# Kernel tuning notes

Hardware: AMD Instinct MI355X
Metric: run time of the kernel (lower is better)

Reference implementation:

```python
import jax, jax.numpy as jnp
from jax import lax
import numpy as np

B, IMG_H, IMG_W = 8, 256, 512
NUM_CLASSES, P = 20, 32
SCALE, TOPK, IOU_THR = 32.0, 100, 0.5


def conv2d(x, w, b, stride=1, pad=1):
    y = lax.conv_general_dilated(x, w, (stride, stride), [(pad, pad), (pad, pad)],
                                 dimension_numbers=('NCHW', 'OIHW', 'NCHW'))
    return y + b[None, :, None, None]


def bilinear_resize(img, out_h, out_w):
    # img: [..., H, W]; torch F.interpolate(mode='bilinear', align_corners=False)
    H, W = img.shape[-2], img.shape[-1]
    def idx_w(n_in, n_out):
        src = (jnp.arange(n_out, dtype=jnp.float32) + 0.5) * (n_in / n_out) - 0.5
        src = jnp.clip(src, 0.0, n_in - 1)
        i0 = jnp.floor(src).astype(jnp.int32)
        i1 = jnp.minimum(i0 + 1, n_in - 1)
        return i0, i1, src - i0.astype(jnp.float32)
    y0, y1, wy = idx_w(H, out_h)
    x0, x1, wx = idx_w(W, out_w)
    top = img[..., y0, :] * (1.0 - wy)[:, None] + img[..., y1, :] * wy[:, None]
    return top[..., x0] * (1.0 - wx) + top[..., x1] * wx


def generate_anchors(fh, fw):
    ys = (jnp.arange(fh, dtype=jnp.float32) + 0.5) * (IMG_H / fh)
    xs = (jnp.arange(fw, dtype=jnp.float32) + 0.5) * (IMG_W / fw)
    cy, cx = jnp.meshgrid(ys, xs, indexing='ij')
    h = SCALE / 2
    return jnp.stack([cx - h, cy - h, cx + h, cy + h], -1).reshape(-1, 4)


def delta_to_boxes(anchors, deltas):
    a_c = (anchors[:, :2] + anchors[:, 2:]) / 2
    a_wh = anchors[:, 2:] - anchors[:, :2]
    pc = a_c + deltas[..., :2] * a_wh
    pwh = a_wh * jnp.exp(deltas[..., 2:])
    return jnp.concatenate([pc - pwh / 2, pc + pwh / 2], -1)


def nms_single(boxes, scores, labels):
    # torchvision batched_nms: offset boxes per label, greedy NMS, return kept idxs
    N = boxes.shape[0]
    off = labels.astype(boxes.dtype) * (jnp.max(boxes) + 1.0)
    b = boxes + off[:, None]
    order = jnp.argsort(-scores)
    bs = b[order]
    area = (bs[:, 2] - bs[:, 0]) * (bs[:, 3] - bs[:, 1])
    lt = jnp.maximum(bs[:, None, :2], bs[None, :, :2])
    rb = jnp.minimum(bs[:, None, 2:], bs[None, :, 2:])
    wh = jnp.clip(rb - lt, 0.0)
    inter = wh[..., 0] * wh[..., 1]
    iou = inter / (area[:, None] + area[None, :] - inter + 1e-9)
    idxs = jnp.arange(N)
    def body(i, suppressed):
        keep_i = jnp.logical_not(suppressed[i])
        row = (iou[i] > IOU_THR) & (idxs > i)
        return jnp.where(keep_i, suppressed | row, suppressed)
    suppressed = lax.fori_loop(0, N, body, jnp.zeros(N, bool))
    keep_mask = ~suppressed
    rank = jnp.cumsum(keep_mask) - 1
    slots = jnp.where(keep_mask & (rank < TOPK), rank, TOPK)
    out = jnp.full(TOPK + 1, -1, jnp.int32).at[slots].set(order.astype(jnp.int32))
    return out[:TOPK]


def setup_inputs():
    key = jax.random.key(0)
    ks = jax.random.split(key, 17)
    def cw(k, o, i, kh, kw_):
        return jax.random.normal(k, (o, i, kh, kw_), jnp.float32) / np.sqrt(i * kh * kw_)
    return {
        'images': jax.random.normal(ks[0], (B, 3, IMG_H, IMG_W), jnp.float32),
        'w1': cw(ks[1], 64, 3, 3, 3),   'b1': jnp.zeros(64, jnp.float32),
        'w2': cw(ks[2], 128, 64, 3, 3), 'b2': jnp.zeros(128, jnp.float32),
        'w3': cw(ks[3], 256, 128, 3, 3),'b3': jnp.zeros(256, jnp.float32),
        'pw1': cw(ks[4], 256, 256, 3, 3), 'pb1': jnp.zeros(256, jnp.float32),
        'pw2': cw(ks[5], P, 256, 1, 1),   'pb2': jnp.zeros(P, jnp.float32),
        'cw_': cw(ks[6], NUM_CLASSES + 1, 256, 3, 3), 'cb': jnp.zeros(NUM_CLASSES + 1, jnp.float32),
        'bw': cw(ks[7], 4, 256, 3, 3),  'bb': jnp.zeros(4, jnp.float32),
        'kw': cw(ks[8], P, 256, 3, 3),  'kb': jnp.zeros(P, jnp.float32),
    }


def reference(images, w1, b1, w2, b2, w3, b3, pw1, pb1, pw2, pb2, cw_, cb, bw, bb, kw, kb):
    x = jax.nn.relu(conv2d(images, w1, b1, stride=2))
    x = jax.nn.relu(conv2d(x, w2, b2, stride=2))
    feat = jax.nn.relu(conv2d(x, w3, b3, stride=2))          # [B,256,32,64]
    proto = conv2d(jax.nn.relu(conv2d(feat, pw1, pb1)), pw2, pb2, pad=0)  # [B,P,32,64]
    fh, fw = feat.shape[2], feat.shape[3]
    def head(w, b, c):
        return conv2d(feat, w, b).transpose(0, 2, 3, 1).reshape(B, -1, c)
    cls = head(cw_, cb, NUM_CLASSES + 1)     # [B,N,C+1]
    box = head(bw, bb, 4)                    # [B,N,4]
    coef = head(kw, kb, P)                   # [B,N,P]
    anchors = generate_anchors(fh, fw)       # [N,4]
    probs = jax.nn.softmax(cls, -1)[..., :-1]
    scores = probs.max(-1)
    labels = probs.argmax(-1).astype(jnp.int32)
    boxes = delta_to_boxes(anchors, box)     # [B,N,4]
    keep = jax.vmap(nms_single)(boxes, scores, labels)   # [B,100], -1 pad
    valid = keep >= 0
    ki = jnp.clip(keep, 0)
    take = lambda a: jnp.take_along_axis(a, ki[..., None] if a.ndim == 3 else ki, axis=1)
    boxes_k = take(boxes) * valid[..., None]
    scores_k = take(scores) * valid
    labels_k = jnp.where(valid, take(labels), 0)
    coef_k = jnp.take_along_axis(coef, ki[..., None], axis=1)   # [B,100,P]
    m = jax.nn.sigmoid(jnp.einsum('bkp,bphw->bkhw', coef_k, proto))
    masks = bilinear_resize(m, IMG_H, IMG_W) > 0.5
    masks = masks & valid[..., None, None]
    return boxes_k, scores_k, labels_k, masks, valid
```

## Files before the change

kernel.cpp:

```cpp
#include <hip/hip_runtime.h>
#include <hip/hip_bf16.h>
#include <math.h>

#define BB 8
#define NCLS 21
#define NANCH 2048
#define TOPK_N 100

static const size_t OFF_X1HI = 0;
static const size_t OFF_X1LO = 34344960;
static const size_t OFF_X2HI = 68689920;
static const size_t OFF_X2LO = 86261760;
static const size_t OFF_FTHI = 103833600;
static const size_t OFF_FTLO = 113025024;
static const size_t ZERO_BYTES = 122216448;
static const size_t OFF_WT1  = 122216448;
static const size_t OFF_A2H  = 122223616;
static const size_t OFF_A2L  = 122371072;
static const size_t OFF_A3H  = 122518528;
static const size_t OFF_A3L  = 123108352;
static const size_t OFF_AHH  = 123698176;
static const size_t OFF_AHL  = 123993088;
static const size_t OFF_AP1H = 124288000;
static const size_t OFF_AP1L = 125467648;
static const size_t OFF_WTP2 = 126647296;
static const size_t OFF_BH   = 126680064;
static const size_t OFF_HOUT = 126680576;
static const size_t OFF_P1   = 130874880;
static const size_t OFF_PROTO= 147652096;
static const size_t OFF_BOXES= 149749248;
static const size_t OFF_SCORES=150011392;
static const size_t OFF_LABELS=150076928;
static const size_t OFF_ORDER= 150142464;
static const size_t OFF_SB   = 150208000;
static const size_t OFF_IOU  = 150470144;
static const size_t OFF_KEEP = 154664448;
static const size_t OFF_MAXB = 154668032;
static const size_t OFF_M    = 154668544;

static const size_t OUT_BOXES  = 0;
static const size_t OUT_SCORES = 3200;
static const size_t OUT_LABELS = 4000;
static const size_t OUT_MASKS  = 4800;
static const size_t OUT_VALID  = 104862400;

typedef __attribute__((ext_vector_type(8))) short bf16x8;
typedef __attribute__((ext_vector_type(4))) float f32x4;

__device__ __forceinline__ unsigned encf(float f){
  unsigned u = __float_as_uint(f);
  return (u & 0x80000000u) ? ~u : (u | 0x80000000u);
}
__device__ __forceinline__ float decf(unsigned u){
  unsigned b = (u & 0x80000000u) ? (u & 0x7fffffffu) : ~u;
  return __uint_as_float(b);
}
__device__ __forceinline__ short f2bf(float f){
  __hip_bfloat16 h = __float2bfloat16(f);
  return *(short*)&h;
}
__device__ __forceinline__ float bf2f(short h){
  return __uint_as_float(((unsigned)(unsigned short)h) << 16);
}

__global__ void zerok(float4* __restrict__ p, long n4, unsigned* __restrict__ maxb){
  long i = (long)blockIdx.x*256 + threadIdx.x;
  if (i < BB) maxb[i] = 0u;
  if (i < n4) p[i] = make_float4(0.f,0.f,0.f,0.f);
}

template<int CIN,int COUT,int KK>
__global__ void packw(const float* __restrict__ w, float* __restrict__ wT){
  int i = blockIdx.x*256 + threadIdx.x;
  if (i >= CIN*KK*COUT) return;
  int co = i % COUT; int r = i / COUT;
  int ci = r / KK,  k = r % KK;
  wT[i] = w[(co*CIN + ci)*KK + k];
}

template<int CIN,int COUT>
__global__ void packA(const float* __restrict__ w, short* __restrict__ Ahi,
                      short* __restrict__ Alo){
  constexpr int K = CIN*9;
  constexpr int KS = K/32;
  int i = blockIdx.x*256 + threadIdx.x;
  if (i >= COUT*K) return;
  int sub  = i & 7;
  int lane = (i >> 3) & 63;
  int rest = i >> 9;
  int ks = rest % KS;
  int mt = rest / KS;
  int m = mt*16 + (lane & 15);
  int k = ks*32 + (lane >> 4)*8 + sub;
  int tap = k / CIN, ci = k - tap*CIN;
  float v = w[(m*CIN + ci)*9 + tap];
  short h = f2bf(v);
  Ahi[i] = h;
  Alo[i] = f2bf(v - bf2f(h));
}

__global__ void packAh(const float* __restrict__ cw, const float* __restrict__ bw,
                       const float* __restrict__ kw, const float* __restrict__ cb,
                       const float* __restrict__ bb, const float* __restrict__ kb,
                       short* __restrict__ Ahi, short* __restrict__ Alo,
                       float* __restrict__ bh){
  int i = blockIdx.x*256 + threadIdx.x;
  if (i < 64){
    float v = 0.f;
    if (i < 21) v = cb[i]; else if (i < 25) v = bb[i-21]; else if (i < 57) v = kb[i-25];
    bh[i] = v;
  }
  if (i >= 64*2304) return;
  constexpr int KS = 72;
  int sub  = i & 7;
  int lane = (i >> 3) & 63;
  int rest = i >> 9;
  int ks = rest % KS;
  int mt = rest / KS;
  int m = mt*16 + (lane & 15);
  int k = ks*32 + (lane >> 4)*8 + sub;
  int tap = k >> 8, ci = k & 255;
  float v = 0.f;
  if (m < 21)      v = cw[(m*256 + ci)*9 + tap];
  else if (m < 25) v = bw[((m-21)*256 + ci)*9 + tap];
  else if (m < 57) v = kw[((m-25)*256 + ci)*9 + tap];
  short h = f2bf(v);
  Ahi[i] = h;
  Alo[i] = f2bf(v - bf2f(h));
}

__global__ __launch_bounds__(256) void conv1k(const float* __restrict__ img,
    const float* __restrict__ wT, const float* __restrict__ bias,
    short* __restrict__ x1hi, short* __restrict__ x1lo){
  const int b   = blockIdx.z;
  const int co0 = blockIdx.y * 16;
  const int g   = blockIdx.x*256 + threadIdx.x;
  const int y  = g >> 7;
  const int x0 = (g & 127) << 1;

  float acc[16][2];
#pragma unroll
  for (int c=0;c<16;c++){
    float bv = bias[co0+c];
    acc[c][0] = bv; acc[c][1] = bv;
  }
  int   off[3][5];
  float msk[3][5];
#pragma unroll
  for (int kh=0;kh<3;kh++){
    int iy = y*2 - 1 + kh;
    bool okr = (iy >= 0) && (iy < 256);
    int ro = okr ? iy*512 : 0;
#pragma unroll
    for (int t=0;t<5;t++){
      int col = x0*2 - 1 + t;
      bool ok = okr && (col >= 0) && (col < 512);
      off[kh][t] = ok ? (ro + col) : 0;
      msk[kh][t] = ok ? 1.f : 0.f;
    }
  }
  const float* inb = img + (size_t)b*3*256*512;
  for (int ci=0; ci<3; ci++){
    const float* inc = inb + (size_t)ci*256*512;
    float v[3][5];
#pragma unroll
    for (int kh=0;kh<3;kh++)
#pragma unroll
      for (int t=0;t<5;t++)
        v[kh][t] = inc[off[kh][t]] * msk[kh][t];
    const float* wp = wT + ci*9*64 + co0;
#pragma unroll
    for (int kh=0;kh<3;kh++)
#pragma unroll
    for (int kw=0;kw<3;kw++){
      const float* wq = wp + (kh*3+kw)*64;
#pragma unroll
      for (int c=0;c<16;c++){
        float wv = wq[c];
        acc[c][0] = fmaf(wv, v[kh][2*0+kw], acc[c][0]);
        acc[c][1] = fmaf(wv, v[kh][2*1+kw], acc[c][1]);
      }
    }
  }
#pragma unroll
  for (int s=0;s<2;s++){
    short hv[16] __attribute__((aligned(16)));
    short lv[16] __attribute__((aligned(16)));
#pragma unroll
    for (int c=0;c<16;c++){
      float r = fmaxf(acc[c][s], 0.f);
      short h = f2bf(r);
      hv[c] = h;
      lv[c] = f2bf(r - bf2f(h));
    }
#pragma unroll
    for (int g2=0; g2<2; g2++){
      size_t ad = (((size_t)(b*8 + (co0>>3) + g2)*130 + (y+1))*258 + (x0+s+1))*8;
      *(bf16x8*)(x1hi + ad) = *(bf16x8*)(hv + g2*8);
      *(bf16x8*)(x1lo + ad) = *(bf16x8*)(lv + g2*8);
    }
  }
}

template<int CIN,int K,int M,int MW,int NW,int OW,int OHh,int S,int IPH,int IPW,
         bool SPLIT,int EMODE,int OPH,int OPW>
__global__ __launch_bounds__(NW*64) void cgemm(
    const short* __restrict__ Ahi, const short* __restrict__ Alo,
    const short* __restrict__ Bhi, const short* __restrict__ Blo,
    const float* __restrict__ bias, float* __restrict__ outf,
    short* __restrict__ outhi, short* __restrict__ outlo){
  static_assert(CIN % 32 == 0, "CIN must be multiple of 32");
  constexpr int NT = OW*OHh;
  constexpr int KS = K/32;
  constexpr int CG = CIN/8;
  const int b    = blockIdx.z;
  const int wave = threadIdx.x >> 6;
  const int lane = threadIdx.x & 63;
  const int lm = lane & 15, lq = lane >> 4;
  const int m0 = (blockIdx.y * NW + wave) * (MW*16);
  const int n0 = blockIdx.x * 64;

  int oy[4], ox[4];
#pragma unroll
  for (int j=0;j<4;j++){
    int n = n0 + j*16 + lm;
    oy[j] = n / OW; ox[j] = n % OW;
  }

  f32x4 acc[MW][4];
#pragma unroll
  for (int i=0;i<MW;i++)
#pragma unroll
    for (int j=0;j<4;j++) acc[i][j] = (f32x4){0.f,0.f,0.f,0.f};

  const short* Ah_l = Ahi + (size_t)lane*8;
  const short* Al_l = Alo + (size_t)lane*8;
  const int mt0 = m0 >> 4;

  const size_t plane = (size_t)IPH*IPW;
  const short* Bh0 = Bhi + ((size_t)b*CG + lq)*plane*8;
  const short* Bl0 = Blo + ((size_t)b*CG + lq)*plane*8;

#pragma unroll 3
  for (int tap=0; tap<9; tap++){
    const int dy = tap/3, dx = tap%3;
    size_t pix[4];
#pragma unroll
    for (int j=0;j<4;j++)
      pix[j] = (size_t)(oy[j]*S + dy)*IPW + (size_t)(ox[j]*S + dx);
    const int ksb = tap*(CIN/32);
#pragma unroll
    for (int kc=0; kc<CIN; kc+=32){
      const int ks = ksb + (kc>>5);
      const size_t koff = (size_t)(kc>>3)*plane;
      bf16x8 ah[MW], bh_[4];
#pragma unroll
      for (int i=0;i<MW;i++)
        ah[i] = *(const bf16x8*)(Ah_l + ((size_t)(mt0+i)*KS + ks)*512);
#pragma unroll
      for (int j=0;j<4;j++) bh_[j] = *(const bf16x8*)(Bh0 + (koff + pix[j])*8);
      if constexpr (SPLIT){
        bf16x8 al[MW], bl_[4];
#pragma unroll
        for (int i=0;i<MW;i++)
          al[i] = *(const bf16x8*)(Al_l + ((size_t)(mt0+i)*KS + ks)*512);
#pragma unroll
        for (int j=0;j<4;j++) bl_[j] = *(const bf16x8*)(Bl0 + (koff + pix[j])*8);
#pragma unroll
        for (int j=0;j<4;j++)
#pragma unroll
          for (int i=0;i<MW;i++)
            acc[i][j] = __builtin_amdgcn_mfma_f32_16x16x32_bf16(ah[i], bh_[j], acc[i][j], 0,0,0);
#pragma unroll
        for (int j=0;j<4;j++)
#pragma unroll
          for (int i=0;i<MW;i++)
            acc[i][j] = __builtin_amdgcn_mfma_f32_16x16x32_bf16(ah[i], bl_[j], acc[i][j], 0,0,0);
#pragma unroll
        for (int j=0;j<4;j++)
#pragma unroll
          for (int i=0;i<MW;i++)
            acc[i][j] = __builtin_amdgcn_mfma_f32_16x16x32_bf16(al[i], bh_[j], acc[i][j], 0,0,0);
      } else {
#pragma unroll
        for (int j=0;j<4;j++)
#pragma unroll
          for (int i=0;i<MW;i++)
            acc[i][j] = __builtin_amdgcn_mfma_f32_16x16x32_bf16(ah[i], bh_[j], acc[i][j], 0,0,0);
      }
    }
  }

#pragma unroll
  for (int i=0;i<MW;i++){
#pragma unroll
    for (int r=0;r<4;r++){
      const int m = m0 + i*16 + lq*4 + r;
      const float bv = bias[m];
      if constexpr (EMODE == 0){
#pragma unroll
        for (int j=0;j<4;j++){
          float v = fmaxf(acc[i][j][r] + bv, 0.f);
          short h = f2bf(v);
          short l = f2bf(v - bf2f(h));
          size_t ad = ((((size_t)(b*(M/8) + (m>>3))*OPH + (oy[j]+1))*OPW + (ox[j]+1)))*8 + (m&7);
          outhi[ad] = h;
          outlo[ad] = l;
        }
      } else {
        float* cp = outf + ((size_t)b*M + m)*NT + n0 + lm;
#pragma unroll
        for (int j=0;j<4;j++){
          float v = acc[i][j][r] + bv;
          if constexpr (EMODE == 2) v = fmaxf(v, 0.f);
          cp[j*16] = v;
        }
      }
    }
  }
}

template<int CIN,int K,int M,int MW,int NW,int S,int IPH,int IPW,
         bool SPLIT,int EMODE,int OPH,int OPW>
__global__ __launch_bounds__(NW*64) void cgemm_row(
    const short* __restrict__ Ahi, const short* __restrict__ Alo,
    const short* __restrict__ Bhi, const short* __restrict__ Blo,
    const float* __restrict__ bias, float* __restrict__ outf,
    short* __restrict__ outhi, short* __restrict__ outlo){
  static_assert(CIN % 32 == 0, "CIN must be multiple of 32");
  constexpr int NT = 64*32;
  constexpr int KS = K/32;
  constexpr int CG = CIN/8;
  __shared__ short sB[CG*IPW*8];

  const int b    = blockIdx.z;
  const int oy   = blockIdx.x;
  const int wave = threadIdx.x >> 6;
  const int lane = threadIdx.x & 63;
  const int lm = lane & 15, lq = lane >> 4;
  const int m0 = (blockIdx.y * NW + wave) * (MW*16);
  const int tid = threadIdx.x;

  int ox[4];
#pragma unroll
  for (int j=0;j<4;j++) ox[j] = j*16 + lm;

  f32x4 acc[MW][4];
#pragma unroll
  for (int i=0;i<MW;i++)
#pragma unroll
    for (int j=0;j<4;j++) acc[i][j] = (f32x4){0.f,0.f,0.f,0.f};

  const short* Ah_l = Ahi + (size_t)lane*8;
  const short* Al_l = Alo + (size_t)lane*8;
  const int mt0 = m0 >> 4;
  const size_t plane = (size_t)IPH*IPW;
  const short* Bl0 = Blo + ((size_t)b*CG + lq)*plane*8;

#pragma unroll 1
  for (int dy=0; dy<3; dy++){
    const int iy = oy*S + dy;
    __syncthreads();
    {
      const short* srch = Bhi + ((size_t)b*CG*IPH + iy)*IPW*8;
      for (int c = tid; c < CG*IPW; c += NW*64){
        int g = c / IPW, p = c - g*IPW;
        *(bf16x8*)(&sB[(g*IPW + p)*8]) =
          *(const bf16x8*)(srch + ((size_t)g*plane + p)*8);
      }
    }
    __syncthreads();
#pragma unroll
    for (int dx=0; dx<3; dx++){
      const int tap = dy*3 + dx;
      const int ksb = tap*(CIN/32);
#pragma unroll
      for (int kc=0; kc<CIN; kc+=32){
        const int ks = ksb + (kc>>5);
        bf16x8 ah[MW], bh_[4];
#pragma unroll
        for (int i=0;i<MW;i++)
          ah[i] = *(const bf16x8*)(Ah_l + ((size_t)(mt0+i)*KS + ks)*512);
#pragma unroll
        for (int j=0;j<4;j++){
          int p = ox[j]*S + dx;
          bh_[j] = *(const bf16x8*)(&sB[(((kc>>3) + lq)*IPW + p)*8]);
        }
        if constexpr (SPLIT){
          const size_t koff = (size_t)(kc>>3)*plane;
          bf16x8 al[MW], bl_[4];
#pragma unroll
          for (int i=0;i<MW;i++)
            al[i] = *(const bf16x8*)(Al_l + ((size_t)(mt0+i)*KS + ks)*512);
#pragma unroll
          for (int j=0;j<4;j++){
            size_t pix = (size_t)iy*IPW + (size_t)(ox[j]*S + dx);
            bl_[j] = *(const bf16x8*)(Bl0 + (koff + pix)*8);
          }
#pragma unroll
          for (int j=0;j<4;j++)
#pragma unroll
            for (int i=0;i<MW;i++)
              acc[i][j] = __builtin_amdgcn_mfma_f32_16x16x32_bf16(ah[i], bh_[j], acc[i][j], 0,0,0);
#pragma unroll
          for (int j=0;j<4;j++)
#pragma unroll
            for (int i=0;i<MW;i++)
              acc[i][j] = __builtin_amdgcn_mfma_f32_16x16x32_bf16(ah[i], bl_[j], acc[i][j], 0,0,0);
#pragma unroll
          for (int j=0;j<4;j++)
#pragma unroll
            for (int i=0;i<MW;i++)
              acc[i][j] = __builtin_amdgcn_mfma_f32_16x16x32_bf16(al[i], bh_[j], acc[i][j], 0,0,0);
        } else {
#pragma unroll
          for (int j=0;j<4;j++)
#pragma unroll
            for (int i=0;i<MW;i++)
              acc[i][j] = __builtin_amdgcn_mfma_f32_16x16x32_bf16(ah[i], bh_[j], acc[i][j], 0,0,0);
        }
      }
    }
  }

#pragma unroll
  for (int i=0;i<MW;i++){
#pragma unroll
    for (int r=0;r<4;r++){
      const int m = m0 + i*16 + lq*4 + r;
      const float bv = bias[m];
      if constexpr (EMODE == 0){
#pragma unroll
        for (int j=0;j<4;j++){
          float v = fmaxf(acc[i][j][r] + bv, 0.f);
          short h = f2bf(v);
          short l = f2bf(v - bf2f(h));
          size_t ad = ((((size_t)(b*(M/8) + (m>>3))*OPH + (oy+1))*OPW + (ox[j]+1)))*8 + (m&7);
          outhi[ad] = h;
          outlo[ad] = l;
        }
      } else {
        float* cp = outf + ((size_t)b*M + m)*NT + oy*64 + lm;
#pragma unroll
        for (int j=0;j<4;j++){
          float v = acc[i][j][r] + bv;
          if constexpr (EMODE == 2) v = fmaxf(v, 0.f);
          cp[j*16] = v;
        }
      }
    }
  }
}

__global__ __launch_bounds__(256) void pw2k2(const float* __restrict__ p1,
    const float* __restrict__ wT, const float* __restrict__ bias,
    float* __restrict__ proto){
  const int b  = blockIdx.y;
  const int sp = blockIdx.x*256 + threadIdx.x;
  float acc[32];
#pragma unroll
  for (int c=0;c<32;c++) acc[c] = bias[c];
  const float* pb = p1 + (size_t)b*256*NANCH + sp;
  for (int ci=0;ci<256;ci++){
    float v = pb[(size_t)ci*NANCH];
    const float* wq = wT + ci*32;
#pragma unroll
    for (int c=0;c<32;c++) acc[c] = fmaf(v, wq[c], acc[c]);
  }
#pragma unroll
  for (int c=0;c<32;c++)
    proto[((size_t)b*32 + c)*NANCH + sp] = acc[c];
}

__global__ void decodek(const float* __restrict__ hout,
                        float* __restrict__ boxes, float* __restrict__ scores,
                        int* __restrict__ labels, unsigned* __restrict__ maxb){
  const int b = blockIdx.y;
  const int n = blockIdx.x*blockDim.x + threadIdx.x;
  const float* cp = hout + (size_t)b*64*NANCH + n;
  float l[NCLS];
  float M = -1e30f;
#pragma unroll
  for (int c=0;c<NCLS;c++){ l[c] = cp[(size_t)c*NANCH]; M = fmaxf(M, l[c]); }
  float denom = 0.f;
#pragma unroll
  for (int c=0;c<NCLS;c++) denom += expf(l[c]-M);
  float best = -1.f; int bi = 0;
#pragma unroll
  for (int c=0;c<NCLS-1;c++){
    float e = expf(l[c]-M);
    if (e > best){ best = e; bi = c; }
  }
  scores[(size_t)b*NANCH + n] = best/denom;
  labels[(size_t)b*NANCH + n] = bi;

  float dx = cp[21*(size_t)NANCH], dy = cp[22*(size_t)NANCH];
  float dw = cp[23*(size_t)NANCH], dh = cp[24*(size_t)NANCH];
  const int yy = n >> 6, xx = n & 63;
  float cx = (xx+0.5f)*8.f, cy = (yy+0.5f)*8.f;
  float px = cx + dx*32.f, py = cy + dy*32.f;
  float pw = 32.f*expf(dw), ph = 32.f*expf(dh);
  float x1 = px - 0.5f*pw, y1 = py - 0.5f*ph;
  float x2 = px + 0.5f*pw, y2 = py + 0.5f*ph;
  float* bo = boxes + ((size_t)b*NANCH + n)*4;
  bo[0]=x1; bo[1]=y1; bo[2]=x2; bo[3]=y2;
  float mx = fmaxf(fmaxf(x1,y1), fmaxf(x2,y2));
#pragma unroll
  for (int off=32; off>0; off>>=1) mx = fmaxf(mx, __shfl_down(mx, off));
  if ((threadIdx.x & 63) == 0) atomicMax(maxb + b, encf(mx));
}

__global__ void __launch_bounds__(1024) sortk(const float* __restrict__ scores,
                     const float* __restrict__ boxes, const int* __restrict__ labels,
                     const unsigned* __restrict__ maxb,
                     int* __restrict__ order, float* __restrict__ sb){
  __shared__ float sc[NANCH];
  __shared__ int   id[NANCH];
  const int b = blockIdx.x, t = threadIdx.x;
  for (int i=t;i<NANCH;i+=1024){ sc[i]=scores[(size_t)b*NANCH+i]; id[i]=i; }
  __syncthreads();
  for (int k=2;k<=NANCH;k<<=1){
    for (int j=k>>1;j>0;j>>=1){
      for (int i=t;i<NANCH;i+=1024){
        int ixj = i ^ j;
        if (ixj > i){
          float sa=sc[i], sb_=sc[ixj]; int ia=id[i], ib=id[ixj];
          bool dir = ((i & k) == 0);
          bool before_ba = (sb_ > sa) || (sb_ == sa && ib < ia);
          if (before_ba == dir){ sc[i]=sb_; sc[ixj]=sa; id[i]=ib; id[ixj]=ia; }
        }
      }
      __syncthreads();
    }
  }
  float mboff = decf(maxb[b]) + 1.0f;
  for (int r=t;r<NANCH;r+=1024){
    int o = id[r];
    order[(size_t)b*NANCH + r] = o;
    float off = (float)labels[(size_t)b*NANCH + o] * mboff;
    const float* bo = boxes + ((size_t)b*NANCH + o)*4;
    float* sp = sb + ((size_t)b*NANCH + r)*4;
    sp[0]=bo[0]+off; sp[1]=bo[1]+off; sp[2]=bo[2]+off; sp[3]=bo[3]+off;
  }
}

__global__ void ioumask(const float* __restrict__ sb, unsigned long long* __restrict__ iou){
  const int b = blockIdx.y;
  const int gid = blockIdx.x*blockDim.x + threadIdx.x;
  const int i = gid >> 5, w = gid & 31;
  const float* base = sb + (size_t)b*NANCH*4;
  unsigned long long bits = 0ull;
  const int j0 = w << 6;
  if (j0 + 63 > i){
    float x1=base[i*4], y1=base[i*4+1], x2=base[i*4+2], y2=base[i*4+3];
    float ai = (x2-x1)*(y2-y1);
    for (int jj=0;jj<64;jj++){
      int j = j0 + jj;
      if (j > i){
        float bx1=base[j*4], by1=base[j*4+1], bx2=base[j*4+2], by2=base[j*4+3];
        float lx=fmaxf(x1,bx1), ly=fmaxf(y1,by1);
        float rx=fminf(x2,bx2), ry=fminf(y2,by2);
        float ww=fmaxf(rx-lx,0.f), hh=fmaxf(ry-ly,0.f);
        float inter = ww*hh;
        float aj = (bx2-bx1)*(by2-by1);
        float v = inter/(ai + aj - inter + 1e-9f);
        if (v > 0.5f) bits |= (1ull << jj);
      }
    }
  }
  iou[((size_t)b*NANCH + i)*32 + w] = bits;
}

__global__ void nmsscan(const unsigned long long* __restrict__ iou,
                        const int* __restrict__ order, int* __restrict__ keep){
  const int b = blockIdx.x, lane = threadIdx.x;
  unsigned long long sup = 0ull;
  int k = 0;
  for (int i=0; i<NANCH && k<TOPK_N; i++){
    int wi = i >> 6, bi = i & 63;
    unsigned long long wv = __shfl(sup, wi);
    if (!((wv >> bi) & 1ull)){
      if (lane == 0) keep[b*TOPK_N + k] = order[(size_t)b*NANCH + i];
      k++;
      unsigned long long row = (lane < 32) ? iou[((size_t)b*NANCH + i)*32 + lane] : 0ull;
      sup |= row;
    }
  }
  for (int r = lane; r < TOPK_N; r += 64)
    if (r >= k) keep[b*TOPK_N + r] = -1;
}

__global__ void gatherk(const int* __restrict__ keep, const float* __restrict__ boxes,
                        const float* __restrict__ scores, const int* __restrict__ labels,
                        float* __restrict__ out){
  const int b = blockIdx.x, r = threadIdx.x;
  if (r >= TOPK_N) return;
  int ki = keep[b*TOPK_N + r];
  float valid = (ki >= 0) ? 1.f : 0.f;
  int kc = (ki < 0) ? 0 : ki;
  const float* bo = boxes + ((size_t)b*NANCH + kc)*4;
#pragma unroll
  for (int c=0;c<4;c++) out[OUT_BOXES + ((size_t)b*TOPK_N + r)*4 + c] = bo[c]*valid;
  out[OUT_SCORES + b*TOPK_N + r] = scores[(size_t)b*NANCH + kc]*valid;
  out[OUT_LABELS + b*TOPK_N + r] = (ki >= 0) ? (float)labels[(size_t)b*NANCH + kc] : 0.f;
  out[OUT_VALID  + b*TOPK_N + r] = valid;
}

__global__ void maskm(const int* __restrict__ keep, const float* __restrict__ hout,
                      const float* __restrict__ proto, float* __restrict__ m){
  const int b = blockIdx.z, r = blockIdx.y;
  const int s = blockIdx.x*blockDim.x + threadIdx.x;
  __shared__ float cf[32];
  int ki = keep[b*TOPK_N + r];
  int kc = (ki < 0) ? 0 : ki;
  if (threadIdx.x < 32)
    cf[threadIdx.x] = hout[((size_t)b*64 + 25 + threadIdx.x)*NANCH + kc];
  __syncthreads();
  float acc = 0.f;
#pragma unroll
  for (int p=0;p<32;p++) acc = fmaf(cf[p], proto[((size_t)b*32 + p)*NANCH + s], acc);
  m[((size_t)b*TOPK_N + r)*NANCH + s] = 1.f/(1.f + expf(-acc));
}

__global__ void resizek(const float* __restrict__ m, const int* __restrict__ keep,
                        float* __restrict__ out){
  const int b = blockIdx.z, r = blockIdx.y;
  const int pid = blockIdx.x*blockDim.x + threadIdx.x;
  const int y  = pid >> 7;
  const int x4 = (pid & 127) << 2;
  bool valid = keep[b*TOPK_N + r] >= 0;
  const float* mb = m + ((size_t)b*TOPK_N + r)*NANCH;
  float sy = (y + 0.5f)*0.125f - 0.5f;
  sy = fminf(fmaxf(sy, 0.f), 31.f);
  int y0 = (int)floorf(sy);
  int y1 = min(y0+1, 31);
  float wy = sy - (float)y0;
  const float* r0 = mb + y0*64;
  const float* r1 = mb + y1*64;
  float res[4];
#pragma unroll
  for (int k=0;k<4;k++){
    int x = x4 + k;
    float sx = (x + 0.5f)*0.125f - 0.5f;
    sx = fminf(fmaxf(sx, 0.f), 63.f);
    int x0 = (int)floorf(sx);
    int x1 = min(x0+1, 63);
    float wx = sx - (float)x0;
    float t0 = r0[x0]*(1.f-wy) + r1[x0]*wy;
    float t1 = r0[x1]*(1.f-wy) + r1[x1]*wy;
    float v  = t0*(1.f-wx) + t1*wx;
    res[k] = (v > 0.5f && valid) ? 1.f : 0.f;
  }
  float4 v4 = make_float4(res[0], res[1], res[2], res[3]);
  *(float4*)(out + OUT_MASKS + (((size_t)b*TOPK_N + r)*256 + y)*512 + x4) = v4;
}

extern "C" void kernel_launch(void* const* d_in, const int* in_sizes, int n_in,
                              void* d_out, int out_size, void* d_ws, size_t ws_size,
                              hipStream_t stream) {
  const float* images=(const float*)d_in[0];
  const float* w1=(const float*)d_in[1];  const float* b1=(const float*)d_in[2];
  const float* w2=(const float*)d_in[3];  const float* b2=(const float*)d_in[4];
  const float* w3=(const float*)d_in[5];  const float* b3=(const float*)d_in[6];
  const float* pw1=(const float*)d_in[7]; const float* pb1=(const float*)d_in[8];
  const float* pw2=(const float*)d_in[9]; const float* pb2=(const float*)d_in[10];
  const float* cw=(const float*)d_in[11]; const float* cb=(const float*)d_in[12];
  const float* bw=(const float*)d_in[13]; const float* bb=(const float*)d_in[14];
  const float* kw=(const float*)d_in[15]; const float* kb=(const float*)d_in[16];
  float* out = (float*)d_out;
  char* ws = (char*)d_ws;

  short* x1hi = (short*)(ws + OFF_X1HI);
  short* x1lo = (short*)(ws + OFF_X1LO);
  short* x2hi = (short*)(ws + OFF_X2HI);
  short* x2lo = (short*)(ws + OFF_X2LO);
  short* fthi = (short*)(ws + OFF_FTHI);
  short* ftlo = (short*)(ws + OFF_FTLO);
  float* wT1  = (float*)(ws + OFF_WT1);
  short* a2h  = (short*)(ws + OFF_A2H);
  short* a2l  = (short*)(ws + OFF_A2L);
  short* a3h  = (short*)(ws + OFF_A3H);
  short* a3l  = (short*)(ws + OFF_A3L);
  short* ahh  = (short*)(ws + OFF_AHH);
  short* ahl  = (short*)(ws + OFF_AHL);
  short* ap1h = (short*)(ws + OFF_AP1H);
  short* ap1l = (short*)(ws + OFF_AP1L);
  float* wTp2 = (float*)(ws + OFF_WTP2);
  float* bh   = (float*)(ws + OFF_BH);
  float* hout = (float*)(ws + OFF_HOUT);
  float* p1   = (float*)(ws + OFF_P1);
  float* proto= (float*)(ws + OFF_PROTO);
  float* boxes= (float*)(ws + OFF_BOXES);
  float* scores=(float*)(ws + OFF_SCORES);
  int*   labels=(int*)  (ws + OFF_LABELS);
  int*   order =(int*)  (ws + OFF_ORDER);
  float* sb   = (float*)(ws + OFF_SB);
  unsigned long long* iou = (unsigned long long*)(ws + OFF_IOU);
  int*   keep = (int*)  (ws + OFF_KEEP);
  unsigned* maxb = (unsigned*)(ws + OFF_MAXB);
  float* m    = (float*)(ws + OFF_M);

  zerok<<<dim3((unsigned)(ZERO_BYTES/16/256)), 256, 0, stream>>>((float4*)ws, (long)(ZERO_BYTES/16), maxb);

  packw<3,64,9>  <<<dim3(7),    256, 0, stream>>>(w1, wT1);
  packA<64,128>  <<<dim3(288),  256, 0, stream>>>(w2, a2h, a2l);
  packA<128,256> <<<dim3(1152), 256, 0, stream>>>(w3, a3h, a3l);
  packA<256,256> <<<dim3(2304), 256, 0, stream>>>(pw1, ap1h, ap1l);
  packAh<<<dim3(576), 256, 0, stream>>>(cw, bw, kw, cb, bb, kb, ahh, ahl, bh);
  packw<256,32,1><<<dim3(32),   256, 0, stream>>>(pw2, wTp2);

  conv1k<<<dim3(64,4,BB), 256, 0, stream>>>(images, wT1, b1, x1hi, x1lo);

  cgemm<64,576,128,2,4,128,64,2,130,258,true,0,66,130>
      <<<dim3(128,1,BB), 256, 0, stream>>>(a2h, a2l, x1hi, x1lo, b2, nullptr, x2hi, x2lo);

  cgemm_row<128,1152,256,2,4,2,66,130,true,0,34,66>
      <<<dim3(32,2,BB), 256, 0, stream>>>(a3h, a3l, x2hi, x2lo, b3, nullptr, fthi, ftlo);

  cgemm_row<256,2304,64,2,2,1,34,66,true,1,1,1>
      <<<dim3(32,1,BB), 128, 0, stream>>>(ahh, ahl, fthi, ftlo, bh, hout, nullptr, nullptr);

  cgemm_row<256,2304,256,2,4,1,34,66,false,2,1,1>
      <<<dim3(32,2,BB), 256, 0, stream>>>(ap1h, ap1l, fthi, fthi, pb1, p1, nullptr, nullptr);

  pw2k2<<<dim3(8,BB), 256, 0, stream>>>(p1, wTp2, pb2, proto);

  decodek<<<dim3(8,BB), 256, 0, stream>>>(hout, boxes, scores, labels, maxb);
  sortk<<<dim3(BB), 1024, 0, stream>>>(scores, boxes, labels, maxb, order, sb);
  ioumask<<<dim3(256,BB), 256, 0, stream>>>(sb, iou);
  nmsscan<<<dim3(BB), 64, 0, stream>>>(iou, order, keep);
  gatherk<<<dim3(BB), 128, 0, stream>>>(keep, boxes, scores, labels, out);

  maskm<<<dim3(8,TOPK_N,BB), 256, 0, stream>>>(keep, hout, proto, m);
  resizek<<<dim3(128,TOPK_N,BB), 256, 0, stream>>>(m, keep, out);
}
```

Measured before the change: 1.004 ms.

## Zero only halos, stage lo planes in LDS, unify conv GEMMs, skip invalid masks

```diff
diff --git a/kernel.cpp b/kernel.cpp
--- a/kernel.cpp
+++ b/kernel.cpp
@@ -13,7 +13,6 @@
 static const size_t OFF_X2LO = 86261760;
 static const size_t OFF_FTHI = 103833600;
 static const size_t OFF_FTLO = 113025024;
-static const size_t ZERO_BYTES = 122216448;
 static const size_t OFF_WT1  = 122216448;
 static const size_t OFF_A2H  = 122223616;
 static const size_t OFF_A2L  = 122371072;
@@ -63,10 +62,22 @@
   return __uint_as_float(((unsigned)(unsigned short)h) << 16);
 }
 
-__global__ void zerok(float4* __restrict__ p, long n4, unsigned* __restrict__ maxb){
-  long i = (long)blockIdx.x*256 + threadIdx.x;
-  if (i < BB) maxb[i] = 0u;
-  if (i < n4) p[i] = make_float4(0.f,0.f,0.f,0.f);
+template<int CH8,int Hp,int Wp>
+__global__ void halok(short* __restrict__ hi, short* __restrict__ lo,
+                      unsigned* __restrict__ maxb){
+  constexpr int PER = 2*Wp + 2*(Hp-2);
+  int i = blockIdx.x*256 + threadIdx.x;
+  if (maxb && i < BB) maxb[i] = 0u;
+  if (i >= BB*CH8*PER) return;
+  int cell = i % PER; int bg = i / PER;
+  int y, x;
+  if (cell < Wp)        { y = 0;      x = cell; }
+  else if (cell < 2*Wp) { y = Hp-1;   x = cell - Wp; }
+  else { int r = cell - 2*Wp; y = 1 + (r>>1); x = (r&1) ? (Wp-1) : 0; }
+  size_t ad = (((size_t)bg*Hp + y)*Wp + x)*8;
+  bf16x8 z = (bf16x8){0,0,0,0,0,0,0,0};
+  *(bf16x8*)(hi + ad) = z;
+  *(bf16x8*)(lo + ad) = z;
 }
 
 template<int CIN,int COUT,int KK>
@@ -202,149 +213,34 @@
   }
 }
 
-template<int CIN,int K,int M,int MW,int NW,int OW,int OHh,int S,int IPH,int IPW,
-         bool SPLIT,int EMODE,int OPH,int OPW>
-__global__ __launch_bounds__(NW*64) void cgemm(
-    const short* __restrict__ Ahi, const short* __restrict__ Alo,
-    const short* __restrict__ Bhi, const short* __restrict__ Blo,
-    const float* __restrict__ bias, float* __restrict__ outf,
-    short* __restrict__ outhi, short* __restrict__ outlo){
-  static_assert(CIN % 32 == 0, "CIN must be multiple of 32");
-  constexpr int NT = OW*OHh;
-  constexpr int KS = K/32;
-  constexpr int CG = CIN/8;
-  const int b    = blockIdx.z;
-  const int wave = threadIdx.x >> 6;
-  const int lane = threadIdx.x & 63;
-  const int lm = lane & 15, lq = lane >> 4;
-  const int m0 = (blockIdx.y * NW + wave) * (MW*16);
-  const int n0 = blockIdx.x * 64;
-
-  int oy[4], ox[4];
-#pragma unroll
-  for (int j=0;j<4;j++){
-    int n = n0 + j*16 + lm;
-    oy[j] = n / OW; ox[j] = n % OW;
-  }
-
-  f32x4 acc[MW][4];
-#pragma unroll
-  for (int i=0;i<MW;i++)
-#pragma unroll
-    for (int j=0;j<4;j++) acc[i][j] = (f32x4){0.f,0.f,0.f,0.f};
-
-  const short* Ah_l = Ahi + (size_t)lane*8;
-  const short* Al_l = Alo + (size_t)lane*8;
-  const int mt0 = m0 >> 4;
-
-  const size_t plane = (size_t)IPH*IPW;
-  const short* Bh0 = Bhi + ((size_t)b*CG + lq)*plane*8;
-  const short* Bl0 = Blo + ((size_t)b*CG + lq)*plane*8;
-
-#pragma unroll 3
-  for (int tap=0; tap<9; tap++){
-    const int dy = tap/3, dx = tap%3;
-    size_t pix[4];
-#pragma unroll
-    for (int j=0;j<4;j++)
-      pix[j] = (size_t)(oy[j]*S + dy)*IPW + (size_t)(ox[j]*S + dx);
-    const int ksb = tap*(CIN/32);
-#pragma unroll
-    for (int kc=0; kc<CIN; kc+=32){
-      const int ks = ksb + (kc>>5);
-      const size_t koff = (size_t)(kc>>3)*plane;
-      bf16x8 ah[MW], bh_[4];
-#pragma unroll
-      for (int i=0;i<MW;i++)
-        ah[i] = *(const bf16x8*)(Ah_l + ((size_t)(mt0+i)*KS + ks)*512);
-#pragma unroll
-      for (int j=0;j<4;j++) bh_[j] = *(const bf16x8*)(Bh0 + (koff + pix[j])*8);
-      if constexpr (SPLIT){
-        bf16x8 al[MW], bl_[4];
-#pragma unroll
-        for (int i=0;i<MW;i++)
-          al[i] = *(const bf16x8*)(Al_l + ((size_t)(mt0+i)*KS + ks)*512);
-#pragma unroll
-        for (int j=0;j<4;j++) bl_[j] = *(const bf16x8*)(Bl0 + (koff + pix[j])*8);
-#pragma unroll
-        for (int j=0;j<4;j++)
-#pragma unroll
-          for (int i=0;i<MW;i++)
-            acc[i][j] = __builtin_amdgcn_mfma_f32_16x16x32_bf16(ah[i], bh_[j], acc[i][j], 0,0,0);
-#pragma unroll
-        for (int j=0;j<4;j++)
-#pragma unroll
-          for (int i=0;i<MW;i++)
-            acc[i][j] = __builtin_amdgcn_mfma_f32_16x16x32_bf16(ah[i], bl_[j], acc[i][j], 0,0,0);
-#pragma unroll
-        for (int j=0;j<4;j++)
-#pragma unroll
-          for (int i=0;i<MW;i++)
-            acc[i][j] = __builtin_amdgcn_mfma_f32_16x16x32_bf16(al[i], bh_[j], acc[i][j], 0,0,0);
-      } else {
-#pragma unroll
-        for (int j=0;j<4;j++)
-#pragma unroll
-          for (int i=0;i<MW;i++)
-            acc[i][j] = __builtin_amdgcn_mfma_f32_16x16x32_bf16(ah[i], bh_[j], acc[i][j], 0,0,0);
-      }
-    }
-  }
-
-#pragma unroll
-  for (int i=0;i<MW;i++){
-#pragma unroll
-    for (int r=0;r<4;r++){
-      const int m = m0 + i*16 + lq*4 + r;
-      const float bv = bias[m];
-      if constexpr (EMODE == 0){
-#pragma unroll
-        for (int j=0;j<4;j++){
-          float v = fmaxf(acc[i][j][r] + bv, 0.f);
-          short h = f2bf(v);
-          short l = f2bf(v - bf2f(h));
-          size_t ad = ((((size_t)(b*(M/8) + (m>>3))*OPH + (oy[j]+1))*OPW + (ox[j]+1)))*8 + (m&7);
-          outhi[ad] = h;
-          outlo[ad] = l;
-        }
-      } else {
-        float* cp = outf + ((size_t)b*M + m)*NT + n0 + lm;
-#pragma unroll
-        for (int j=0;j<4;j++){
-          float v = acc[i][j][r] + bv;
-          if constexpr (EMODE == 2) v = fmaxf(v, 0.f);
-          cp[j*16] = v;
-        }
-      }
-    }
-  }
-}
-
-template<int CIN,int K,int M,int MW,int NW,int S,int IPH,int IPW,
-         bool SPLIT,int EMODE,int OPH,int OPW>
+template<int CIN,int K,int M,int MW,int NW,int S,int IPH,int IPW,int NXB,
+         bool SPLIT,bool STAGELO,int EMODE,int OPH,int OPW>
 __global__ __launch_bounds__(NW*64) void cgemm_row(
     const short* __restrict__ Ahi, const short* __restrict__ Alo,
     const short* __restrict__ Bhi, const short* __restrict__ Blo,
     const float* __restrict__ bias, float* __restrict__ outf,
     short* __restrict__ outhi, short* __restrict__ outlo){
   static_assert(CIN % 32 == 0, "CIN must be multiple of 32");
+  static_assert(EMODE == 0 || NXB == 1, "flat out assumes OW=64");
   constexpr int NT = 64*32;
   constexpr int KS = K/32;
   constexpr int CG = CIN/8;
-  __shared__ short sB[CG*IPW*8];
+  constexpr int SW  = 64*S + 2;
+  constexpr int SWP = (S==2) ? (SW/2 + 1) : SW;
+  constexpr int PARS = (S==2) ? 2 : 1;
+  constexpr int LOOFF = CG*PARS*SWP*8;
+  constexpr int BUFS = (SPLIT && STAGELO) ? 2 : 1;
+  __shared__ __align__(16) short sB[BUFS*LOOFF];
 
   const int b    = blockIdx.z;
-  const int oy   = blockIdx.x;
+  const int oy   = blockIdx.x / NXB;
+  const int xb   = (blockIdx.x % NXB) * 64;
   const int wave = threadIdx.x >> 6;
   const int lane = threadIdx.x & 63;
   const int lm = lane & 15, lq = lane >> 4;
   const int m0 = (blockIdx.y * NW + wave) * (MW*16);
   const int tid = threadIdx.x;
 
-  int ox[4];
-#pragma unroll
-  for (int j=0;j<4;j++) ox[j] = j*16 + lm;
-
   f32x4 acc[MW][4];
 #pragma unroll
   for (int i=0;i<MW;i++)
@@ -362,11 +258,21 @@
     const int iy = oy*S + dy;
     __syncthreads();
     {
-      const short* srch = Bhi + ((size_t)b*CG*IPH + iy)*IPW*8;
-      for (int c = tid; c < CG*IPW; c += NW*64){
-        int g = c / IPW, p = c - g*IPW;
-        *(bf16x8*)(&sB[(g*IPW + p)*8]) =
+      const short* srch = Bhi + (((size_t)b*CG*IPH + iy)*IPW + (size_t)(xb*S))*8;
+      for (int c = tid; c < CG*SW; c += NW*64){
+        int g = c / SW, p = c - g*SW;
+        int dst = (S==2) ? ((g*2 + (p&1))*SWP + (p>>1)) : (g*SW + p);
+        *(bf16x8*)(&sB[(size_t)dst*8]) =
           *(const bf16x8*)(srch + ((size_t)g*plane + p)*8);
+      }
+      if constexpr (SPLIT && STAGELO){
+        const short* srcl = Blo + (((size_t)b*CG*IPH + iy)*IPW + (size_t)(xb*S))*8;
+        for (int c = tid; c < CG*SW; c += NW*64){
+          int g = c / SW, p = c - g*SW;
+          int dst = (S==2) ? ((g*2 + (p&1))*SWP + (p>>1)) : (g*SW + p);
+          *(bf16x8*)(&sB[LOOFF + (size_t)dst*8]) =
+            *(const bf16x8*)(srcl + ((size_t)g*plane + p)*8);
+        }
       }
     }
     __syncthreads();
@@ -374,28 +280,37 @@
     for (int dx=0; dx<3; dx++){
       const int tap = dy*3 + dx;
       const int ksb = tap*(CIN/32);
-#pragma unroll
       for (int kc=0; kc<CIN; kc+=32){
         const int ks = ksb + (kc>>5);
+        int ra[4];
+#pragma unroll
+        for (int j=0;j<4;j++){
+          int pc = (j*16 + lm)*S + dx;
+          ra[j] = (S==2) ? ((((kc>>3) + lq)*2 + (pc&1))*SWP + (pc>>1))
+                         : (((kc>>3) + lq)*SW + pc);
+        }
         bf16x8 ah[MW], bh_[4];
 #pragma unroll
         for (int i=0;i<MW;i++)
           ah[i] = *(const bf16x8*)(Ah_l + ((size_t)(mt0+i)*KS + ks)*512);
 #pragma unroll
-        for (int j=0;j<4;j++){
-          int p = ox[j]*S + dx;
-          bh_[j] = *(const bf16x8*)(&sB[(((kc>>3) + lq)*IPW + p)*8]);
-        }
+        for (int j=0;j<4;j++)
+          bh_[j] = *(const bf16x8*)(&sB[(size_t)ra[j]*8]);
         if constexpr (SPLIT){
-          const size_t koff = (size_t)(kc>>3)*plane;
           bf16x8 al[MW], bl_[4];
 #pragma unroll
           for (int i=0;i<MW;i++)
             al[i] = *(const bf16x8*)(Al_l + ((size_t)(mt0+i)*KS + ks)*512);
-#pragma unroll
-          for (int j=0;j<4;j++){
-            size_t pix = (size_t)iy*IPW + (size_t)(ox[j]*S + dx);
-            bl_[j] = *(const bf16x8*)(Bl0 + (koff + pix)*8);
+          if constexpr (STAGELO){
+#pragma unroll
+            for (int j=0;j<4;j++)
+              bl_[j] = *(const bf16x8*)(&sB[LOOFF + (size_t)ra[j]*8]);
+          } else {
+#pragma unroll
+            for (int j=0;j<4;j++){
+              size_t pix = (size_t)iy*IPW + (size_t)((xb + j*16 + lm)*S + dx);
+              bl_[j] = *(const bf16x8*)(Bl0 + ((size_t)(kc>>3)*plane + pix)*8);
+            }
           }
 #pragma unroll
           for (int j=0;j<4;j++)
@@ -432,10 +347,11 @@
       if constexpr (EMODE == 0){
 #pragma unroll
         for (int j=0;j<4;j++){
+          const int ox = xb + j*16 + lm;
           float v = fmaxf(acc[i][j][r] + bv, 0.f);
           short h = f2bf(v);
           short l = f2bf(v - bf2f(h));
-          size_t ad = ((((size_t)(b*(M/8) + (m>>3))*OPH + (oy+1))*OPW + (ox[j]+1)))*8 + (m&7);
+          size_t ad = ((((size_t)(b*(M/8) + (m>>3))*OPH + (oy+1))*OPW + (ox+1)))*8 + (m&7);
           outhi[ad] = h;
           outlo[ad] = l;
         }
@@ -609,12 +525,12 @@
 __global__ void maskm(const int* __restrict__ keep, const float* __restrict__ hout,
                       const float* __restrict__ proto, float* __restrict__ m){
   const int b = blockIdx.z, r = blockIdx.y;
+  int ki = keep[b*TOPK_N + r];
+  if (ki < 0) return;
   const int s = blockIdx.x*blockDim.x + threadIdx.x;
   __shared__ float cf[32];
-  int ki = keep[b*TOPK_N + r];
-  int kc = (ki < 0) ? 0 : ki;
   if (threadIdx.x < 32)
-    cf[threadIdx.x] = hout[((size_t)b*64 + 25 + threadIdx.x)*NANCH + kc];
+    cf[threadIdx.x] = hout[((size_t)b*64 + 25 + threadIdx.x)*NANCH + ki];
   __syncthreads();
   float acc = 0.f;
 #pragma unroll
@@ -628,7 +544,12 @@
   const int pid = blockIdx.x*blockDim.x + threadIdx.x;
   const int y  = pid >> 7;
   const int x4 = (pid & 127) << 2;
+  float* dst = out + OUT_MASKS + (((size_t)b*TOPK_N + r)*256 + y)*512 + x4;
   bool valid = keep[b*TOPK_N + r] >= 0;
+  if (!valid){
+    *(float4*)dst = make_float4(0.f,0.f,0.f,0.f);
+    return;
+  }
   const float* mb = m + ((size_t)b*TOPK_N + r)*NANCH;
   float sy = (y + 0.5f)*0.125f - 0.5f;
   sy = fminf(fmaxf(sy, 0.f), 31.f);
@@ -649,10 +570,9 @@
     float t0 = r0[x0]*(1.f-wy) + r1[x0]*wy;
     float t1 = r0[x1]*(1.f-wy) + r1[x1]*wy;
     float v  = t0*(1.f-wx) + t1*wx;
-    res[k] = (v > 0.5f && valid) ? 1.f : 0.f;
-  }
-  float4 v4 = make_float4(res[0], res[1], res[2], res[3]);
-  *(float4*)(out + OUT_MASKS + (((size_t)b*TOPK_N + r)*256 + y)*512 + x4) = v4;
+    res[k] = (v > 0.5f) ? 1.f : 0.f;
+  }
+  *(float4*)dst = make_float4(res[0], res[1], res[2], res[3]);
 }
 
 extern "C" void kernel_launch(void* const* d_in, const int* in_sizes, int n_in,
@@ -700,7 +620,9 @@
   unsigned* maxb = (unsigned*)(ws + OFF_MAXB);
   float* m    = (float*)(ws + OFF_M);
 
-  zerok<<<dim3((unsigned)(ZERO_BYTES/16/256)), 256, 0, stream>>>((float4*)ws, (long)(ZERO_BYTES/16), maxb);
+  halok<8,130,258><<<dim3(193), 256, 0, stream>>>(x1hi, x1lo, maxb);
+  halok<16,66,130><<<dim3(194), 256, 0, stream>>>(x2hi, x2lo, nullptr);
+  halok<32,34,66> <<<dim3(196), 256, 0, stream>>>(fthi, ftlo, nullptr);
 
   packw<3,64,9>  <<<dim3(7),    256, 0, stream>>>(w1, wT1);
   packA<64,128>  <<<dim3(288),  256, 0, stream>>>(w2, a2h, a2l);
@@ -711,16 +633,16 @@
 
   conv1k<<<dim3(64,4,BB), 256, 0, stream>>>(images, wT1, b1, x1hi, x1lo);
 
-  cgemm<64,576,128,2,4,128,64,2,130,258,true,0,66,130>
+  cgemm_row<64,576,128,2,4,2,130,258,2,true,true,0,66,130>
       <<<dim3(128,1,BB), 256, 0, stream>>>(a2h, a2l, x1hi, x1lo, b2, nullptr, x2hi, x2lo);
 
-  cgemm_row<128,1152,256,2,4,2,66,130,true,0,34,66>
+  cgemm_row<128,1152,256,2,4,2,66,130,1,true,true,0,34,66>
       <<<dim3(32,2,BB), 256, 0, stream>>>(a3h, a3l, x2hi, x2lo, b3, nullptr, fthi, ftlo);
 
-  cgemm_row<256,2304,64,2,2,1,34,66,true,1,1,1>
-      <<<dim3(32,1,BB), 128, 0, stream>>>(ahh, ahl, fthi, ftlo, bh, hout, nullptr, nullptr);
-
-  cgemm_row<256,2304,256,2,4,1,34,66,false,2,1,1>
+  cgemm_row<256,2304,64,1,4,1,34,66,1,true,true,1,1,1>
+      <<<dim3(32,1,BB), 256, 0, stream>>>(ahh, ahl, fthi, ftlo, bh, hout, nullptr, nullptr);
+
+  cgemm_row<256,2304,256,2,4,1,34,66,1,false,false,2,1,1>
       <<<dim3(32,2,BB), 256, 0, stream>>>(ap1h, ap1l, fthi, fthi, pb1, p1, nullptr, nullptr);
 
   pw2k2<<<dim3(8,BB), 256, 0, stream>>>(p1, wTp2, pb2, proto);
```

Measured after the change: 960.6 us. -4.4%, faster.
